# Performance work log

Measured on AMD Instinct MI355X. Metric: run time of the kernel, lower is better.

The kernel has to match this reference:

```python
import jax, jax.numpy as jnp
import numpy as np


def conv1x1(x, W, b):
    # x: [B,C,H,W], W: [O,C], b: [O]  (torch Conv2d 1x1 squeezed)
    return jnp.einsum('oc,bchw->bohw', W, x) + b[None, :, None, None]


def setup_inputs() -> dict:
    key = jax.random.key(0)
    ks = jax.random.split(key, 7)
    B, C, H, W = 8, 256, 32, 32
    s = 1.0 / np.sqrt(C)
    x = jax.random.normal(ks[0], (B, C, H, W), jnp.float32)
    Wq = jax.random.normal(ks[1], (C, C), jnp.float32) * s
    bq = jax.random.normal(ks[2], (C,), jnp.float32) * 0.01
    Wk = jax.random.normal(ks[3], (C, C), jnp.float32) * s
    bk = jax.random.normal(ks[4], (C,), jnp.float32) * 0.01
    Wo = jax.random.normal(ks[5], (C, C), jnp.float32) * s
    bo = jax.random.normal(ks[6], (C,), jnp.float32) * 0.01
    return {"x": x, "Wq": Wq, "bq": bq, "Wk": Wk, "bk": bk, "Wo": Wo, "bo": bo}


def reference(x, Wq, bq, Wk, bk, Wo, bo):
    B, C, H, W = x.shape
    HW = H * W
    scale = 1.0 / (C ** 0.5)
    # proj_query: torch does view(B,C,HW).permute(0,2,1).transpose(1,2).contiguous().view(-1,C)
    # which is a row-major reshape of [B,C,HW] into [B*HW, C] (channel/spatial interleaved).
    # Reproduced faithfully.
    q = conv1x1(x, Wq, bq).reshape(B, C, HW).reshape(-1, C)          # [B*HW, C]
    # proj_key: view(B,C,HW).transpose(0,1).contiguous().view(C,-1) -> true [C, B*HW]
    k = jnp.transpose(conv1x1(x, Wk, bk).reshape(B, C, HW), (1, 0, 2)).reshape(C, -1)
    x_w = (q @ k).reshape(B * HW, B, HW)                              # [BHW, B, HW]
    out_co = jnp.max(x_w, axis=-1) + jnp.mean(x_w, axis=-1)           # [BHW, B]
    x_co = jnp.mean(out_co, axis=-1).reshape(B, HW) * scale           # [B, HW]
    x_co = jax.nn.softmax(x_co, axis=-1).reshape(B, 1, H, W)
    return conv1x1(x * x_co, Wo, bo)
```

## Files before the change

### kernel.cpp

```cpp
#include <hip/hip_runtime.h>

#define BATCH 8
#define CH 256
#define HWSZ 1024
#define BHW 8192

typedef _Float16 f16;
typedef _Float16 f16x4 __attribute__((ext_vector_type(4)));
typedef _Float16 f16x8 __attribute__((ext_vector_type(8)));
typedef float f32x4 __attribute__((ext_vector_type(4)));
typedef unsigned long long u64;
typedef __attribute__((address_space(3))) unsigned int lds_u32;
typedef __attribute__((address_space(1))) const unsigned int glob_u32;

__global__ __launch_bounds__(256) void xmean_kernel(const float* __restrict__ x,
                                                    float* __restrict__ xmean)
{
    const int row  = blockIdx.x * 16 + (threadIdx.x >> 4);
    const int part = threadIdx.x & 15;
    const float4* p = (const float4*)(x + (size_t)row * HWSZ + part * 64);
    float s = 0.f;
#pragma unroll
    for (int i = 0; i < 16; ++i) { float4 v = p[i]; s += v.x + v.y + v.z + v.w; }
    s += __shfl_xor(s, 1, 64);
    s += __shfl_xor(s, 2, 64);
    s += __shfl_xor(s, 4, 64);
    s += __shfl_xor(s, 8, 64);
    if (part == 0) xmean[row] = s * (1.0f / HWSZ);
}

__global__ __launch_bounds__(256) void kmeanW_kernel(
    const float* __restrict__ Wk, const float* __restrict__ bk,
    const float* __restrict__ xmean, float* __restrict__ kmean)
{
    __shared__ float xm[BATCH * CH];
    const int tid = threadIdx.x;
#pragma unroll
    for (int i = 0; i < 8; ++i) xm[i * 256 + tid] = xmean[i * 256 + tid];
    __syncthreads();

    float acc[8];
#pragma unroll
    for (int b = 0; b < 8; ++b) acc[b] = 0.f;
    const float4* w = (const float4*)(Wk + tid * CH);
    for (int c4 = 0; c4 < 64; ++c4) {
        float4 wv = w[c4];
        float wa[4] = {wv.x, wv.y, wv.z, wv.w};
#pragma unroll
        for (int cc = 0; cc < 4; ++cc)
#pragma unroll
            for (int b = 0; b < 8; ++b)
                acc[b] = fmaf(wa[cc], xm[b * 256 + c4 * 4 + cc], acc[b]);
    }
    const float bkv = bk[tid];
#pragma unroll
    for (int b = 0; b < 8; ++b) kmean[b * 256 + tid] = acc[b] + bkv;
}

__global__ __launch_bounds__(256, 2) void pgemm_kernel(
    const float* __restrict__ x,
    const float* __restrict__ Wq, const float* __restrict__ Wk, const float* __restrict__ Wo,
    const float* __restrict__ bq, const float* __restrict__ bk,
    f16* __restrict__ Qh, char* __restrict__ Ksw, float* __restrict__ Yout)
{
    __shared__ __align__(16) char kbuf[32 * 1024];
    __shared__ __align__(16) float xt[256][36];
    f16* tile = (f16*)&xt[0][0];
    char* tileb = (char*)&xt[0][0];

    const int mb   = blockIdx.y;
    const int pxg0 = blockIdx.x * 32;
    const int b    = pxg0 >> 10;
    const int hw0  = pxg0 & 1023;
    const int tid  = threadIdx.x;
    const int lane = tid & 63;
    const int wid  = tid >> 6;
    const int m = lane & 15, g = lane >> 4;

    {
        const int f4 = tid & 7;
        const int cs = tid >> 3;
#pragma unroll
        for (int pass = 0; pass < 8; ++pass) {
            const int c = pass * 32 + cs;
            float4 v = *(const float4*)(x + ((size_t)b * CH + c) * HWSZ + hw0 + f4 * 4);
            *(float4*)&xt[c][f4 * 4] = v;
        }
    }
    __syncthreads();

    {
        const int px = tid & 31;
        const int q8 = tid >> 5;
        const int sw = (px & 7) << 4;
#pragma unroll
        for (int r = 0; r < 4; ++r) {
            f16x8 hi, lo;
#pragma unroll
            for (int i = 0; i < 8; ++i) {
                const int c = q8 * 32 + r * 8 + i;
                float v = xt[c][px];
                f16 h = (f16)v;
                hi[i] = h;
                lo[i] = (f16)(v - (float)h);
            }
            const int base = q8 * 64 + r * 16;
            *(f16x8*)(kbuf + px * 1024 + (base ^ sw)) = hi;
            *(f16x8*)(kbuf + px * 1024 + 512 + (base ^ sw)) = lo;
        }
    }

    const float* Wsel = (mb == 0) ? Wq : (mb == 1) ? Wk : Wo;
    f16x8 a[4][8];
#pragma unroll
    for (int t = 0; t < 4; ++t)
#pragma unroll
        for (int kk = 0; kk < 8; ++kk) {
            const float* wrow = Wsel + (size_t)(wid * 64 + t * 16 + m) * CH + kk * 32 + g * 8;
            float4 w0 = *(const float4*)(wrow);
            float4 w1 = *(const float4*)(wrow + 4);
            f16x8 av;
            av[0] = (f16)w0.x; av[1] = (f16)w0.y; av[2] = (f16)w0.z; av[3] = (f16)w0.w;
            av[4] = (f16)w1.x; av[5] = (f16)w1.y; av[6] = (f16)w1.z; av[7] = (f16)w1.w;
            a[t][kk] = av;
        }

    __syncthreads();

    f32x4 acc[4][2];
    const f32x4 vz = {0.f, 0.f, 0.f, 0.f};
#pragma unroll
    for (int t = 0; t < 4; ++t) { acc[t][0] = vz; acc[t][1] = vz; }

    const int sw0 = (m & 7) << 4;
#pragma unroll
    for (int ks = 0; ks < 16; ++ks) {
        const int X = ks * 64 + g * 16;
        f16x8 b0 = *(const f16x8*)(kbuf + m * 1024 + (X ^ sw0));
        f16x8 b1 = *(const f16x8*)(kbuf + (16 + m) * 1024 + (X ^ sw0));
#pragma unroll
        for (int t = 0; t < 4; ++t) {
            acc[t][0] = __builtin_amdgcn_mfma_f32_16x16x32_f16(a[t][ks & 7], b0, acc[t][0], 0, 0, 0);
            acc[t][1] = __builtin_amdgcn_mfma_f32_16x16x32_f16(a[t][ks & 7], b1, acc[t][1], 0, 0, 0);
        }
    }

    if (mb == 2) {
#pragma unroll
        for (int t = 0; t < 4; ++t)
#pragma unroll
            for (int u = 0; u < 2; ++u)
#pragma unroll
                for (int j = 0; j < 4; ++j) {
                    const int co = wid * 64 + t * 16 + 4 * g + j;
                    Yout[((size_t)b * CH + co) * HWSZ + hw0 + u * 16 + m] = acc[t][u][j];
                }
        return;
    }

    const float* bias = (mb == 0) ? bq : bk;
    if (mb == 0) {
#pragma unroll
        for (int t = 0; t < 4; ++t) {
            const int co0 = wid * 64 + t * 16 + 4 * g;
            float4 bv = *(const float4*)(bias + co0);
            float ba[4] = {bv.x, bv.y, bv.z, bv.w};
#pragma unroll
            for (int u = 0; u < 2; ++u) {
                const int px = u * 16 + m;
#pragma unroll
                for (int j = 0; j < 4; ++j)
                    tile[(co0 + j) * 32 + (px ^ (j << 3))] = (f16)(acc[t][u][j] + ba[j]);
            }
        }
        __syncthreads();
#pragma unroll
        for (int pass = 0; pass < 4; ++pass) {
            const int co  = pass * 64 + (tid >> 2);
            const int run = tid & 3;
            f16x8 v = *(const f16x8*)(tile + co * 32 + ((run * 8) ^ ((co & 3) << 3)));
            *(f16x8*)(Qh + ((size_t)b * CH + co) * HWSZ + hw0 + run * 8) = v;
        }
    } else {
#pragma unroll
        for (int t = 0; t < 4; ++t) {
            const int co0 = wid * 64 + t * 16 + 4 * g;
            float4 bv = *(const float4*)(bias + co0);
            float ba[4] = {bv.x, bv.y, bv.z, bv.w};
#pragma unroll
            for (int u = 0; u < 2; ++u) {
                const int px = u * 16 + m;
                f16x4 pk;
#pragma unroll
                for (int j = 0; j < 4; ++j) pk[j] = (f16)(acc[t][u][j] + ba[j]);
                *(f16x4*)(tileb + px * 512 + ((co0 * 2) ^ (m << 3))) = pk;
            }
        }
        __syncthreads();
        const int px = tid & 31;
        const int rp = tid >> 5;
        const int kloc = (px & 15) << 3;
        const int kglb = (px & 7) << 4;
        char* grow = Ksw + (size_t)(pxg0 + px) * 512;
#pragma unroll
        for (int i = 0; i < 4; ++i) {
            const int r = rp + i * 8;
            u64 a0 = *(const u64*)(tileb + px * 512 + ((r * 16) ^ kloc));
            u64 a1 = *(const u64*)(tileb + px * 512 + ((r * 16 + 8) ^ kloc));
            char* gdst = grow + ((r * 16) ^ kglb);
            *(u64*)gdst = a0;
            *(u64*)(gdst + 8) = a1;
        }
    }
}

__global__ __launch_bounds__(512, 4) void score_kernel(
    const f16* __restrict__ Qh, const char* __restrict__ Ksw, float* __restrict__ rowmax)
{
    __shared__ __align__(16) char kbuf[2][32768];
    __shared__ float lds_rm[128][2];

    const int batch = blockIdx.x & 7;
    const int r0    = (blockIdx.x >> 3) * 128;
    const int tid   = threadIdx.x;
    const int lane  = tid & 63;
    const int wid   = tid >> 6;
    const int wr = wid >> 1, wc = wid & 1;
    const int m = lane & 15, g = lane >> 4;
    const int rbase = r0 + wr * 32;

    const char* kbase = Ksw + (size_t)batch * HWSZ * 512;

#define STAGE(buf, ch)                                                                  \
    {                                                                                   \
        const char* _src = kbase + (ch) * 64 * 512 + tid * 16;                          \
        char* _dst = &kbuf[buf][tid * 16];                                              \
        __builtin_amdgcn_global_load_lds((glob_u32*)(_src),        (lds_u32*)(_dst),        16, 0, 0); \
        __builtin_amdgcn_global_load_lds((glob_u32*)(_src + 8192), (lds_u32*)(_dst + 8192), 16, 0, 0); \
        __builtin_amdgcn_global_load_lds((glob_u32*)(_src + 16384),(lds_u32*)(_dst + 16384),16, 0, 0); \
        __builtin_amdgcn_global_load_lds((glob_u32*)(_src + 24576),(lds_u32*)(_dst + 24576),16, 0, 0); \
    }

    STAGE(0, 0);

    f16x8 a[2][8];
#pragma unroll
    for (int t = 0; t < 2; ++t)
#pragma unroll
        for (int kk = 0; kk < 8; ++kk)
            a[t][kk] = *(const f16x8*)(Qh + (size_t)(rbase + t * 16 + m) * CH + kk * 32 + 8 * g);

    int boff[8][2];
    {
        const int sw = (m & 7) << 4;
#pragma unroll
        for (int kk = 0; kk < 8; ++kk)
#pragma unroll
            for (int u2 = 0; u2 < 2; ++u2) {
                const int col = wc * 32 + u2 * 16 + m;
                boff[kk][u2] = col * 512 + ((kk * 64 + g * 16) ^ sw);
            }
    }

    float rm[2][4];
#pragma unroll
    for (int t = 0; t < 2; ++t)
#pragma unroll
        for (int jj = 0; jj < 4; ++jj) rm[t][jj] = -1e30f;

    __syncthreads();

    int cur = 0;
    for (int ch = 0; ch < 16; ++ch) {
        if (ch < 15) STAGE(cur ^ 1, ch + 1);

        const char* kb = &kbuf[cur][0];
        f32x4 acc[2][2];
        const f32x4 vz = {0.f, 0.f, 0.f, 0.f};
#pragma unroll
        for (int t = 0; t < 2; ++t) { acc[t][0] = vz; acc[t][1] = vz; }

#pragma unroll
        for (int kk = 0; kk < 8; ++kk) {
            f16x8 bfr[2];
            bfr[0] = *(const f16x8*)(kb + boff[kk][0]);
            bfr[1] = *(const f16x8*)(kb + boff[kk][1]);
#pragma unroll
            for (int t = 0; t < 2; ++t) {
                acc[t][0] = __builtin_amdgcn_mfma_f32_16x16x32_f16(a[t][kk], bfr[0], acc[t][0], 0, 0, 0);
                acc[t][1] = __builtin_amdgcn_mfma_f32_16x16x32_f16(a[t][kk], bfr[1], acc[t][1], 0, 0, 0);
            }
        }

#pragma unroll
        for (int t = 0; t < 2; ++t)
#pragma unroll
            for (int jj = 0; jj < 4; ++jj)
                rm[t][jj] = fmaxf(rm[t][jj], fmaxf(acc[t][0][jj], acc[t][1][jj]));

        __syncthreads();
        cur ^= 1;
    }
#undef STAGE

#pragma unroll
    for (int d = 1; d < 16; d <<= 1)
#pragma unroll
        for (int t = 0; t < 2; ++t)
#pragma unroll
            for (int jj = 0; jj < 4; ++jj)
                rm[t][jj] = fmaxf(rm[t][jj], __shfl_xor(rm[t][jj], d, 64));

    if (m == 0) {
#pragma unroll
        for (int t = 0; t < 2; ++t)
#pragma unroll
            for (int jj = 0; jj < 4; ++jj)
                lds_rm[wr * 32 + t * 16 + g * 4 + jj][wc] = rm[t][jj];
    }
    __syncthreads();
    if (tid < 128)
        rowmax[(size_t)(r0 + tid) * BATCH + batch] = fmaxf(lds_rm[tid][0], lds_rm[tid][1]);
}

__global__ __launch_bounds__(256) void logits_kernel(
    const f16* __restrict__ Qh, const float* __restrict__ kmean,
    const float* __restrict__ rowmax, float* __restrict__ logits)
{
    __shared__ float km[BATCH][CH];
    const int tid = threadIdx.x;
#pragma unroll
    for (int i = 0; i < 8; ++i) km[i][tid] = kmean[i * 256 + tid];
    __syncthreads();

    const int r = blockIdx.x * 256 + tid;
    float acc[8];
#pragma unroll
    for (int b = 0; b < 8; ++b) acc[b] = 0.f;

    const f16x8* q = (const f16x8*)(Qh + (size_t)r * CH);
    for (int c8 = 0; c8 < 32; ++c8) {
        f16x8 qv = q[c8];
        float qf[8];
#pragma unroll
        for (int i = 0; i < 8; ++i) qf[i] = (float)qv[i];
#pragma unroll
        for (int b = 0; b < 8; ++b) {
            float4 k0 = *(const float4*)&km[b][c8 * 8];
            float4 k1 = *(const float4*)&km[b][c8 * 8 + 4];
            acc[b] = fmaf(qf[0], k0.x, acc[b]); acc[b] = fmaf(qf[1], k0.y, acc[b]);
            acc[b] = fmaf(qf[2], k0.z, acc[b]); acc[b] = fmaf(qf[3], k0.w, acc[b]);
            acc[b] = fmaf(qf[4], k1.x, acc[b]); acc[b] = fmaf(qf[5], k1.y, acc[b]);
            acc[b] = fmaf(qf[6], k1.z, acc[b]); acc[b] = fmaf(qf[7], k1.w, acc[b]);
        }
    }
    float lg = 0.f;
#pragma unroll
    for (int b = 0; b < 8; ++b) lg += rowmax[(size_t)r * 8 + b] + acc[b];
    logits[r] = lg * (1.0f / 128.0f);
}

__global__ __launch_bounds__(256) void softmax_kernel(const float* __restrict__ logits,
                                                      float* __restrict__ wgt)
{
    const int br = blockIdx.x, tid = threadIdx.x;
    __shared__ float red[256];
    float l[4];
#pragma unroll
    for (int i = 0; i < 4; ++i) l[i] = logits[br * HWSZ + i * 256 + tid];

    float mx = fmaxf(fmaxf(l[0], l[1]), fmaxf(l[2], l[3]));
    red[tid] = mx;
    __syncthreads();
    for (int s = 128; s > 0; s >>= 1) {
        if (tid < s) red[tid] = fmaxf(red[tid], red[tid + s]);
        __syncthreads();
    }
    mx = red[0];
    __syncthreads();

    float e[4], sm = 0.f;
#pragma unroll
    for (int i = 0; i < 4; ++i) { e[i] = expf(l[i] - mx); sm += e[i]; }
    red[tid] = sm;
    __syncthreads();
    for (int s = 128; s > 0; s >>= 1) {
        if (tid < s) red[tid] += red[tid + s];
        __syncthreads();
    }
    const float inv = 1.0f / red[0];
#pragma unroll
    for (int i = 0; i < 4; ++i)
        wgt[br * HWSZ + i * 256 + tid] = e[i] * inv;
}

__global__ __launch_bounds__(256) void gate_kernel(float* __restrict__ out,
                                                   const float* __restrict__ wgt,
                                                   const float* __restrict__ bo)
{
    const size_t idx = ((size_t)blockIdx.x * 256 + threadIdx.x) * 8;
    const int b  = (int)(idx >> 18);
    const int c  = (int)(idx >> 10) & 255;
    const int hw = (int)idx & 1023;

    float4 y0 = *(const float4*)(out + idx);
    float4 y1 = *(const float4*)(out + idx + 4);
    float4 w0 = *(const float4*)(wgt + b * HWSZ + hw);
    float4 w1 = *(const float4*)(wgt + b * HWSZ + hw + 4);
    const float bov = bo[c];

    float4 o0, o1;
    o0.x = fmaf(y0.x, w0.x, bov); o0.y = fmaf(y0.y, w0.y, bov);
    o0.z = fmaf(y0.z, w0.z, bov); o0.w = fmaf(y0.w, w0.w, bov);
    o1.x = fmaf(y1.x, w1.x, bov); o1.y = fmaf(y1.y, w1.y, bov);
    o1.z = fmaf(y1.z, w1.z, bov); o1.w = fmaf(y1.w, w1.w, bov);
    *(float4*)(out + idx)     = o0;
    *(float4*)(out + idx + 4) = o1;
}

extern "C" void kernel_launch(void* const* d_in, const int* in_sizes, int n_in,
                              void* d_out, int out_size, void* d_ws, size_t ws_size,
                              hipStream_t stream)
{
    const float* x  = (const float*)d_in[0];
    const float* Wq = (const float*)d_in[1];
    const float* bq = (const float*)d_in[2];
    const float* Wk = (const float*)d_in[3];
    const float* bk = (const float*)d_in[4];
    const float* Wo = (const float*)d_in[5];
    const float* bo = (const float*)d_in[6];
    float* out = (float*)d_out;

    char* ws = (char*)d_ws;
    f16*   Qh     = (f16*)(ws);
    char*  Ksw    = (char*)(ws + (4 << 20));
    float* rowmax = (float*)(ws + (8 << 20));
    float* kmean  = (float*)(ws + (8 << 20) + (256 << 10));
    float* xmean  = (float*)(ws + (8 << 20) + (264 << 10));
    float* logits = (float*)(ws + (8 << 20) + (272 << 10));
    float* wgt    = (float*)(ws + (8 << 20) + (304 << 10));

    xmean_kernel  <<<dim3(128),     256, 0, stream>>>(x, xmean);
    kmeanW_kernel <<<dim3(1),       256, 0, stream>>>(Wk, bk, xmean, kmean);
    pgemm_kernel  <<<dim3(256, 3),  256, 0, stream>>>(x, Wq, Wk, Wo, bq, bk, Qh, Ksw, out);
    score_kernel  <<<dim3(512),     512, 0, stream>>>(Qh, Ksw, rowmax);
    logits_kernel <<<dim3(32),      256, 0, stream>>>(Qh, kmean, rowmax, logits);
    softmax_kernel<<<dim3(8),       256, 0, stream>>>(logits, wgt);
    gate_kernel   <<<dim3(1024),    256, 0, stream>>>(out, wgt, bo);
}
```

Baseline: 104.5 us.

## Split projection GEMMs, fuse gate into Wo GEMM, retile score kernel

The Wo projection is moved out of the shared projection kernel into a separate kernel that runs after the softmax and applies the gate weight and bias in its epilogue. This removes the separate read-modify-write gate pass over the output, and that GEMM uses only hi fp16 x with a single K pass. The Q and K projections now share one 512-thread block that converts x once and runs two passes. Other changes: the score kernel goes from 512 to 256 threads with 64 rows per wave-row, xmean uses 32 lanes per row, and kmeanW is spread over 8 blocks.

```diff
diff --git a/kernel.cpp b/kernel.cpp
--- a/kernel.cpp
+++ b/kernel.cpp
@@ -16,16 +16,17 @@
 __global__ __launch_bounds__(256) void xmean_kernel(const float* __restrict__ x,
                                                     float* __restrict__ xmean)
 {
-    const int row  = blockIdx.x * 16 + (threadIdx.x >> 4);
-    const int part = threadIdx.x & 15;
-    const float4* p = (const float4*)(x + (size_t)row * HWSZ + part * 64);
+    const int row  = blockIdx.x * 8 + (threadIdx.x >> 5);
+    const int part = threadIdx.x & 31;
+    const float4* p = (const float4*)(x + (size_t)row * HWSZ);
     float s = 0.f;
 #pragma unroll
-    for (int i = 0; i < 16; ++i) { float4 v = p[i]; s += v.x + v.y + v.z + v.w; }
+    for (int i = 0; i < 8; ++i) { float4 v = p[i * 32 + part]; s += v.x + v.y + v.z + v.w; }
     s += __shfl_xor(s, 1, 64);
     s += __shfl_xor(s, 2, 64);
     s += __shfl_xor(s, 4, 64);
     s += __shfl_xor(s, 8, 64);
+    s += __shfl_xor(s, 16, 64);
     if (part == 0) xmean[row] = s * (1.0f / HWSZ);
 }
 
@@ -33,42 +34,35 @@
     const float* __restrict__ Wk, const float* __restrict__ bk,
     const float* __restrict__ xmean, float* __restrict__ kmean)
 {
-    __shared__ float xm[BATCH * CH];
+    __shared__ float xm[CH];
+    const int b = blockIdx.x;
     const int tid = threadIdx.x;
-#pragma unroll
-    for (int i = 0; i < 8; ++i) xm[i * 256 + tid] = xmean[i * 256 + tid];
-    __syncthreads();
-
-    float acc[8];
-#pragma unroll
-    for (int b = 0; b < 8; ++b) acc[b] = 0.f;
+    xm[tid] = xmean[b * 256 + tid];
+    __syncthreads();
+
+    float acc = 0.f;
     const float4* w = (const float4*)(Wk + tid * CH);
     for (int c4 = 0; c4 < 64; ++c4) {
         float4 wv = w[c4];
-        float wa[4] = {wv.x, wv.y, wv.z, wv.w};
-#pragma unroll
-        for (int cc = 0; cc < 4; ++cc)
-#pragma unroll
-            for (int b = 0; b < 8; ++b)
-                acc[b] = fmaf(wa[cc], xm[b * 256 + c4 * 4 + cc], acc[b]);
-    }
-    const float bkv = bk[tid];
-#pragma unroll
-    for (int b = 0; b < 8; ++b) kmean[b * 256 + tid] = acc[b] + bkv;
-}
-
-__global__ __launch_bounds__(256, 2) void pgemm_kernel(
+        acc = fmaf(wv.x, xm[c4 * 4 + 0], acc);
+        acc = fmaf(wv.y, xm[c4 * 4 + 1], acc);
+        acc = fmaf(wv.z, xm[c4 * 4 + 2], acc);
+        acc = fmaf(wv.w, xm[c4 * 4 + 3], acc);
+    }
+    kmean[b * 256 + tid] = acc + bk[tid];
+}
+
+__global__ __launch_bounds__(512, 1) void pgemmQK_kernel(
     const float* __restrict__ x,
-    const float* __restrict__ Wq, const float* __restrict__ Wk, const float* __restrict__ Wo,
+    const float* __restrict__ Wq, const float* __restrict__ Wk,
     const float* __restrict__ bq, const float* __restrict__ bk,
-    f16* __restrict__ Qh, char* __restrict__ Ksw, float* __restrict__ Yout)
+    f16* __restrict__ Qh, char* __restrict__ Ksw)
 {
     __shared__ __align__(16) char kbuf[32 * 1024];
     __shared__ __align__(16) float xt[256][36];
     f16* tile = (f16*)&xt[0][0];
     char* tileb = (char*)&xt[0][0];
 
-    const int mb   = blockIdx.y;
     const int pxg0 = blockIdx.x * 32;
     const int b    = pxg0 >> 10;
     const int hw0  = pxg0 & 1023;
@@ -81,8 +75,8 @@
         const int f4 = tid & 7;
         const int cs = tid >> 3;
 #pragma unroll
-        for (int pass = 0; pass < 8; ++pass) {
-            const int c = pass * 32 + cs;
+        for (int pass = 0; pass < 4; ++pass) {
+            const int c = pass * 64 + cs;
             float4 v = *(const float4*)(x + ((size_t)b * CH + c) * HWSZ + hw0 + f4 * 4);
             *(float4*)&xt[c][f4 * 4] = v;
         }
@@ -94,117 +88,115 @@
         const int q8 = tid >> 5;
         const int sw = (px & 7) << 4;
 #pragma unroll
-        for (int r = 0; r < 4; ++r) {
+        for (int r = 0; r < 2; ++r) {
             f16x8 hi, lo;
 #pragma unroll
             for (int i = 0; i < 8; ++i) {
-                const int c = q8 * 32 + r * 8 + i;
+                const int c = q8 * 16 + r * 8 + i;
                 float v = xt[c][px];
                 f16 h = (f16)v;
                 hi[i] = h;
                 lo[i] = (f16)(v - (float)h);
             }
-            const int base = q8 * 64 + r * 16;
+            const int base = q8 * 32 + r * 16;
             *(f16x8*)(kbuf + px * 1024 + (base ^ sw)) = hi;
             *(f16x8*)(kbuf + px * 1024 + 512 + (base ^ sw)) = lo;
         }
     }
 
-    const float* Wsel = (mb == 0) ? Wq : (mb == 1) ? Wk : Wo;
-    f16x8 a[4][8];
-#pragma unroll
-    for (int t = 0; t < 4; ++t)
-#pragma unroll
-        for (int kk = 0; kk < 8; ++kk) {
-            const float* wrow = Wsel + (size_t)(wid * 64 + t * 16 + m) * CH + kk * 32 + g * 8;
-            float4 w0 = *(const float4*)(wrow);
-            float4 w1 = *(const float4*)(wrow + 4);
-            f16x8 av;
-            av[0] = (f16)w0.x; av[1] = (f16)w0.y; av[2] = (f16)w0.z; av[3] = (f16)w0.w;
-            av[4] = (f16)w1.x; av[5] = (f16)w1.y; av[6] = (f16)w1.z; av[7] = (f16)w1.w;
-            a[t][kk] = av;
-        }
-
-    __syncthreads();
-
-    f32x4 acc[4][2];
+    f16x8 a[2][8];
+#define LOAD_W(Wsel)                                                                     \
+    {                                                                                    \
+        _Pragma("unroll")                                                                \
+        for (int t = 0; t < 2; ++t)                                                      \
+            _Pragma("unroll")                                                            \
+            for (int kk = 0; kk < 8; ++kk) {                                             \
+                const float* wrow = (Wsel) + (size_t)(wid * 32 + t * 16 + m) * CH + kk * 32 + g * 8; \
+                float4 w0 = *(const float4*)(wrow);                                      \
+                float4 w1 = *(const float4*)(wrow + 4);                                  \
+                f16x8 av;                                                                \
+                av[0] = (f16)w0.x; av[1] = (f16)w0.y; av[2] = (f16)w0.z; av[3] = (f16)w0.w; \
+                av[4] = (f16)w1.x; av[5] = (f16)w1.y; av[6] = (f16)w1.z; av[7] = (f16)w1.w; \
+                a[t][kk] = av;                                                           \
+            }                                                                            \
+    }
+    LOAD_W(Wq);
+    __syncthreads();
+
+    const int sw0 = (m & 7) << 4;
     const f32x4 vz = {0.f, 0.f, 0.f, 0.f};
-#pragma unroll
-    for (int t = 0; t < 4; ++t) { acc[t][0] = vz; acc[t][1] = vz; }
-
-    const int sw0 = (m & 7) << 4;
-#pragma unroll
-    for (int ks = 0; ks < 16; ++ks) {
-        const int X = ks * 64 + g * 16;
-        f16x8 b0 = *(const f16x8*)(kbuf + m * 1024 + (X ^ sw0));
-        f16x8 b1 = *(const f16x8*)(kbuf + (16 + m) * 1024 + (X ^ sw0));
-#pragma unroll
-        for (int t = 0; t < 4; ++t) {
-            acc[t][0] = __builtin_amdgcn_mfma_f32_16x16x32_f16(a[t][ks & 7], b0, acc[t][0], 0, 0, 0);
-            acc[t][1] = __builtin_amdgcn_mfma_f32_16x16x32_f16(a[t][ks & 7], b1, acc[t][1], 0, 0, 0);
-        }
-    }
-
-    if (mb == 2) {
-#pragma unroll
-        for (int t = 0; t < 4; ++t)
-#pragma unroll
-            for (int u = 0; u < 2; ++u)
-#pragma unroll
-                for (int j = 0; j < 4; ++j) {
-                    const int co = wid * 64 + t * 16 + 4 * g + j;
-                    Yout[((size_t)b * CH + co) * HWSZ + hw0 + u * 16 + m] = acc[t][u][j];
-                }
-        return;
-    }
-
-    const float* bias = (mb == 0) ? bq : bk;
-    if (mb == 0) {
-#pragma unroll
-        for (int t = 0; t < 4; ++t) {
-            const int co0 = wid * 64 + t * 16 + 4 * g;
-            float4 bv = *(const float4*)(bias + co0);
-            float ba[4] = {bv.x, bv.y, bv.z, bv.w};
-#pragma unroll
-            for (int u = 0; u < 2; ++u) {
-                const int px = u * 16 + m;
-#pragma unroll
-                for (int j = 0; j < 4; ++j)
-                    tile[(co0 + j) * 32 + (px ^ (j << 3))] = (f16)(acc[t][u][j] + ba[j]);
-            }
-        }
-        __syncthreads();
-#pragma unroll
-        for (int pass = 0; pass < 4; ++pass) {
-            const int co  = pass * 64 + (tid >> 2);
-            const int run = tid & 3;
-            f16x8 v = *(const f16x8*)(tile + co * 32 + ((run * 8) ^ ((co & 3) << 3)));
-            *(f16x8*)(Qh + ((size_t)b * CH + co) * HWSZ + hw0 + run * 8) = v;
-        }
-    } else {
-#pragma unroll
-        for (int t = 0; t < 4; ++t) {
-            const int co0 = wid * 64 + t * 16 + 4 * g;
-            float4 bv = *(const float4*)(bias + co0);
-            float ba[4] = {bv.x, bv.y, bv.z, bv.w};
-#pragma unroll
-            for (int u = 0; u < 2; ++u) {
-                const int px = u * 16 + m;
-                f16x4 pk;
-#pragma unroll
-                for (int j = 0; j < 4; ++j) pk[j] = (f16)(acc[t][u][j] + ba[j]);
-                *(f16x4*)(tileb + px * 512 + ((co0 * 2) ^ (m << 3))) = pk;
-            }
-        }
-        __syncthreads();
+    f32x4 acc[2][2];
+
+#define MFMA_PASS()                                                                      \
+    {                                                                                    \
+        _Pragma("unroll")                                                                \
+        for (int t = 0; t < 2; ++t) { acc[t][0] = vz; acc[t][1] = vz; }                  \
+        _Pragma("unroll")                                                                \
+        for (int ks = 0; ks < 16; ++ks) {                                                \
+            const int X = ks * 64 + g * 16;                                              \
+            f16x8 b0 = *(const f16x8*)(kbuf + m * 1024 + (X ^ sw0));                     \
+            f16x8 b1 = *(const f16x8*)(kbuf + (16 + m) * 1024 + (X ^ sw0));              \
+            _Pragma("unroll")                                                            \
+            for (int t = 0; t < 2; ++t) {                                                \
+                acc[t][0] = __builtin_amdgcn_mfma_f32_16x16x32_f16(a[t][ks & 7], b0, acc[t][0], 0, 0, 0); \
+                acc[t][1] = __builtin_amdgcn_mfma_f32_16x16x32_f16(a[t][ks & 7], b1, acc[t][1], 0, 0, 0); \
+            }                                                                            \
+        }                                                                                \
+    }
+
+    MFMA_PASS();
+
+#pragma unroll
+    for (int t = 0; t < 2; ++t) {
+        const int co0 = wid * 32 + t * 16 + 4 * g;
+        float4 bv = *(const float4*)(bq + co0);
+        float ba[4] = {bv.x, bv.y, bv.z, bv.w};
+#pragma unroll
+        for (int u = 0; u < 2; ++u) {
+            const int px = u * 16 + m;
+#pragma unroll
+            for (int j = 0; j < 4; ++j)
+                tile[(co0 + j) * 32 + (px ^ (j << 3))] = (f16)(acc[t][u][j] + ba[j]);
+        }
+    }
+    __syncthreads();
+#pragma unroll
+    for (int pass = 0; pass < 2; ++pass) {
+        const int co  = pass * 128 + (tid >> 2);
+        const int run = tid & 3;
+        f16x8 v = *(const f16x8*)(tile + co * 32 + ((run * 8) ^ ((co & 3) << 3)));
+        *(f16x8*)(Qh + ((size_t)b * CH + co) * HWSZ + hw0 + run * 8) = v;
+    }
+
+    LOAD_W(Wk);
+    MFMA_PASS();
+    __syncthreads();
+
+#pragma unroll
+    for (int t = 0; t < 2; ++t) {
+        const int co0 = wid * 32 + t * 16 + 4 * g;
+        float4 bv = *(const float4*)(bk + co0);
+        float ba[4] = {bv.x, bv.y, bv.z, bv.w};
+#pragma unroll
+        for (int u = 0; u < 2; ++u) {
+            const int px = u * 16 + m;
+            f16x4 pk;
+#pragma unroll
+            for (int j = 0; j < 4; ++j) pk[j] = (f16)(acc[t][u][j] + ba[j]);
+            *(f16x4*)(tileb + px * 512 + ((co0 * 2) ^ (m << 3)));
+            *(f16x4*)(tileb + px * 512 + ((co0 * 2) ^ (m << 3))) = pk;
+        }
+    }
+    __syncthreads();
+    {
         const int px = tid & 31;
         const int rp = tid >> 5;
         const int kloc = (px & 15) << 3;
         const int kglb = (px & 7) << 4;
         char* grow = Ksw + (size_t)(pxg0 + px) * 512;
 #pragma unroll
-        for (int i = 0; i < 4; ++i) {
-            const int r = rp + i * 8;
+        for (int i = 0; i < 2; ++i) {
+            const int r = rp + i * 16;
             u64 a0 = *(const u64*)(tileb + px * 512 + ((r * 16) ^ kloc));
             u64 a1 = *(const u64*)(tileb + px * 512 + ((r * 16 + 8) ^ kloc));
             char* gdst = grow + ((r * 16) ^ kglb);
@@ -212,9 +204,11 @@
             *(u64*)(gdst + 8) = a1;
         }
     }
-}
-
-__global__ __launch_bounds__(512, 4) void score_kernel(
+#undef MFMA_PASS
+#undef LOAD_W
+}
+
+__global__ __launch_bounds__(256, 2) void score_kernel(
     const f16* __restrict__ Qh, const char* __restrict__ Ksw, float* __restrict__ rowmax)
 {
     __shared__ __align__(16) char kbuf[2][32768];
@@ -227,25 +221,25 @@
     const int wid   = tid >> 6;
     const int wr = wid >> 1, wc = wid & 1;
     const int m = lane & 15, g = lane >> 4;
-    const int rbase = r0 + wr * 32;
+    const int rbase = r0 + wr * 64;
 
     const char* kbase = Ksw + (size_t)batch * HWSZ * 512;
 
-#define STAGE(buf, ch)                                                                  \
-    {                                                                                   \
-        const char* _src = kbase + (ch) * 64 * 512 + tid * 16;                          \
-        char* _dst = &kbuf[buf][tid * 16];                                              \
-        __builtin_amdgcn_global_load_lds((glob_u32*)(_src),        (lds_u32*)(_dst),        16, 0, 0); \
-        __builtin_amdgcn_global_load_lds((glob_u32*)(_src + 8192), (lds_u32*)(_dst + 8192), 16, 0, 0); \
-        __builtin_amdgcn_global_load_lds((glob_u32*)(_src + 16384),(lds_u32*)(_dst + 16384),16, 0, 0); \
-        __builtin_amdgcn_global_load_lds((glob_u32*)(_src + 24576),(lds_u32*)(_dst + 24576),16, 0, 0); \
+#define STAGE(buf, ch)                                                                   \
+    {                                                                                    \
+        const char* _src = kbase + (ch) * 64 * 512 + tid * 16;                           \
+        char* _dst = &kbuf[buf][tid * 16];                                               \
+        _Pragma("unroll")                                                                \
+        for (int k = 0; k < 8; ++k)                                                      \
+            __builtin_amdgcn_global_load_lds((glob_u32*)(_src + k * 4096),               \
+                                             (lds_u32*)(_dst + k * 4096), 16, 0, 0);     \
     }
 
     STAGE(0, 0);
 
-    f16x8 a[2][8];
-#pragma unroll
-    for (int t = 0; t < 2; ++t)
+    f16x8 a[4][8];
+#pragma unroll
+    for (int t = 0; t < 4; ++t)
 #pragma unroll
         for (int kk = 0; kk < 8; ++kk)
             a[t][kk] = *(const f16x8*)(Qh + (size_t)(rbase + t * 16 + m) * CH + kk * 32 + 8 * g);
@@ -262,9 +256,9 @@
             }
     }
 
-    float rm[2][4];
-#pragma unroll
-    for (int t = 0; t < 2; ++t)
+    float rm[4][4];
+#pragma unroll
+    for (int t = 0; t < 4; ++t)
 #pragma unroll
         for (int jj = 0; jj < 4; ++jj) rm[t][jj] = -1e30f;
 
@@ -275,10 +269,10 @@
         if (ch < 15) STAGE(cur ^ 1, ch + 1);
 
         const char* kb = &kbuf[cur][0];
-        f32x4 acc[2][2];
+        f32x4 acc[4][2];
         const f32x4 vz = {0.f, 0.f, 0.f, 0.f};
 #pragma unroll
-        for (int t = 0; t < 2; ++t) { acc[t][0] = vz; acc[t][1] = vz; }
+        for (int t = 0; t < 4; ++t) { acc[t][0] = vz; acc[t][1] = vz; }
 
 #pragma unroll
         for (int kk = 0; kk < 8; ++kk) {
@@ -286,14 +280,14 @@
             bfr[0] = *(const f16x8*)(kb + boff[kk][0]);
             bfr[1] = *(const f16x8*)(kb + boff[kk][1]);
 #pragma unroll
-            for (int t = 0; t < 2; ++t) {
+            for (int t = 0; t < 4; ++t) {
                 acc[t][0] = __builtin_amdgcn_mfma_f32_16x16x32_f16(a[t][kk], bfr[0], acc[t][0], 0, 0, 0);
                 acc[t][1] = __builtin_amdgcn_mfma_f32_16x16x32_f16(a[t][kk], bfr[1], acc[t][1], 0, 0, 0);
             }
         }
 
 #pragma unroll
-        for (int t = 0; t < 2; ++t)
+        for (int t = 0; t < 4; ++t)
 #pragma unroll
             for (int jj = 0; jj < 4; ++jj)
                 rm[t][jj] = fmaxf(rm[t][jj], fmaxf(acc[t][0][jj], acc[t][1][jj]));
@@ -306,17 +300,17 @@
 #pragma unroll
     for (int d = 1; d < 16; d <<= 1)
 #pragma unroll
-        for (int t = 0; t < 2; ++t)
+        for (int t = 0; t < 4; ++t)
 #pragma unroll
             for (int jj = 0; jj < 4; ++jj)
                 rm[t][jj] = fmaxf(rm[t][jj], __shfl_xor(rm[t][jj], d, 64));
 
     if (m == 0) {
 #pragma unroll
-        for (int t = 0; t < 2; ++t)
+        for (int t = 0; t < 4; ++t)
 #pragma unroll
             for (int jj = 0; jj < 4; ++jj)
-                lds_rm[wr * 32 + t * 16 + g * 4 + jj][wc] = rm[t][jj];
+                lds_rm[wr * 64 + t * 16 + g * 4 + jj][wc] = rm[t][jj];
     }
     __syncthreads();
     if (tid < 128)
@@ -394,28 +388,96 @@
         wgt[br * HWSZ + i * 256 + tid] = e[i] * inv;
 }
 
-__global__ __launch_bounds__(256) void gate_kernel(float* __restrict__ out,
-                                                   const float* __restrict__ wgt,
-                                                   const float* __restrict__ bo)
-{
-    const size_t idx = ((size_t)blockIdx.x * 256 + threadIdx.x) * 8;
-    const int b  = (int)(idx >> 18);
-    const int c  = (int)(idx >> 10) & 255;
-    const int hw = (int)idx & 1023;
-
-    float4 y0 = *(const float4*)(out + idx);
-    float4 y1 = *(const float4*)(out + idx + 4);
-    float4 w0 = *(const float4*)(wgt + b * HWSZ + hw);
-    float4 w1 = *(const float4*)(wgt + b * HWSZ + hw + 4);
-    const float bov = bo[c];
-
-    float4 o0, o1;
-    o0.x = fmaf(y0.x, w0.x, bov); o0.y = fmaf(y0.y, w0.y, bov);
-    o0.z = fmaf(y0.z, w0.z, bov); o0.w = fmaf(y0.w, w0.w, bov);
-    o1.x = fmaf(y1.x, w1.x, bov); o1.y = fmaf(y1.y, w1.y, bov);
-    o1.z = fmaf(y1.z, w1.z, bov); o1.w = fmaf(y1.w, w1.w, bov);
-    *(float4*)(out + idx)     = o0;
-    *(float4*)(out + idx + 4) = o1;
+__global__ __launch_bounds__(512, 1) void pgemmY_kernel(
+    const float* __restrict__ x, const float* __restrict__ Wo, const float* __restrict__ bo,
+    const float* __restrict__ wgt, float* __restrict__ out)
+{
+    __shared__ __align__(16) char kbuf[16 * 1024];
+    __shared__ __align__(16) float xt[256][36];
+
+    const int pxg0 = blockIdx.x * 32;
+    const int b    = pxg0 >> 10;
+    const int hw0  = pxg0 & 1023;
+    const int tid  = threadIdx.x;
+    const int lane = tid & 63;
+    const int wid  = tid >> 6;
+    const int m = lane & 15, g = lane >> 4;
+
+    {
+        const int f4 = tid & 7;
+        const int cs = tid >> 3;
+#pragma unroll
+        for (int pass = 0; pass < 4; ++pass) {
+            const int c = pass * 64 + cs;
+            float4 v = *(const float4*)(x + ((size_t)b * CH + c) * HWSZ + hw0 + f4 * 4);
+            *(float4*)&xt[c][f4 * 4] = v;
+        }
+    }
+    __syncthreads();
+
+    {
+        const int px = tid & 31;
+        const int q8 = tid >> 5;
+        const int sw = (px & 7) << 4;
+#pragma unroll
+        for (int r = 0; r < 2; ++r) {
+            f16x8 hi;
+#pragma unroll
+            for (int i = 0; i < 8; ++i)
+                hi[i] = (f16)xt[q8 * 16 + r * 8 + i][px];
+            *(f16x8*)(kbuf + px * 512 + ((q8 * 32 + r * 16) ^ sw)) = hi;
+        }
+    }
+
+    f16x8 a[2][8];
+#pragma unroll
+    for (int t = 0; t < 2; ++t)
+#pragma unroll
+        for (int kk = 0; kk < 8; ++kk) {
+            const float* wrow = Wo + (size_t)(wid * 32 + t * 16 + m) * CH + kk * 32 + g * 8;
+            float4 w0 = *(const float4*)(wrow);
+            float4 w1 = *(const float4*)(wrow + 4);
+            f16x8 av;
+            av[0] = (f16)w0.x; av[1] = (f16)w0.y; av[2] = (f16)w0.z; av[3] = (f16)w0.w;
+            av[4] = (f16)w1.x; av[5] = (f16)w1.y; av[6] = (f16)w1.z; av[7] = (f16)w1.w;
+            a[t][kk] = av;
+        }
+
+    __syncthreads();
+
+    f32x4 acc[2][2];
+    const f32x4 vz = {0.f, 0.f, 0.f, 0.f};
+#pragma unroll
+    for (int t = 0; t < 2; ++t) { acc[t][0] = vz; acc[t][1] = vz; }
+
+    const int sw0 = (m & 7) << 4;
+#pragma unroll
+    for (int ks = 0; ks < 8; ++ks) {
+        const int X = ks * 64 + g * 16;
+        f16x8 b0 = *(const f16x8*)(kbuf + m * 512 + (X ^ sw0));
+        f16x8 b1 = *(const f16x8*)(kbuf + (16 + m) * 512 + (X ^ sw0));
+#pragma unroll
+        for (int t = 0; t < 2; ++t) {
+            acc[t][0] = __builtin_amdgcn_mfma_f32_16x16x32_f16(a[t][ks], b0, acc[t][0], 0, 0, 0);
+            acc[t][1] = __builtin_amdgcn_mfma_f32_16x16x32_f16(a[t][ks], b1, acc[t][1], 0, 0, 0);
+        }
+    }
+
+    float wv[2];
+    wv[0] = wgt[b * HWSZ + hw0 + m];
+    wv[1] = wgt[b * HWSZ + hw0 + 16 + m];
+#pragma unroll
+    for (int t = 0; t < 2; ++t) {
+        const int co0 = wid * 32 + t * 16 + 4 * g;
+        float4 bv = *(const float4*)(bo + co0);
+        float ba[4] = {bv.x, bv.y, bv.z, bv.w};
+#pragma unroll
+        for (int u = 0; u < 2; ++u)
+#pragma unroll
+            for (int j = 0; j < 4; ++j)
+                out[((size_t)b * CH + co0 + j) * HWSZ + hw0 + u * 16 + m] =
+                    fmaf(acc[t][u][j], wv[u], ba[j]);
+    }
 }
 
 extern "C" void kernel_launch(void* const* d_in, const int* in_sizes, int n_in,
@@ -440,11 +502,11 @@
     float* logits = (float*)(ws + (8 << 20) + (272 << 10));
     float* wgt    = (float*)(ws + (8 << 20) + (304 << 10));
 
-    xmean_kernel  <<<dim3(128),     256, 0, stream>>>(x, xmean);
-    kmeanW_kernel <<<dim3(1),       256, 0, stream>>>(Wk, bk, xmean, kmean);
-    pgemm_kernel  <<<dim3(256, 3),  256, 0, stream>>>(x, Wq, Wk, Wo, bq, bk, Qh, Ksw, out);
-    score_kernel  <<<dim3(512),     512, 0, stream>>>(Qh, Ksw, rowmax);
-    logits_kernel <<<dim3(32),      256, 0, stream>>>(Qh, kmean, rowmax, logits);
-    softmax_kernel<<<dim3(8),       256, 0, stream>>>(logits, wgt);
-    gate_kernel   <<<dim3(1024),    256, 0, stream>>>(out, wgt, bo);
-}
+    xmean_kernel  <<<dim3(256),  256, 0, stream>>>(x, xmean);
+    kmeanW_kernel <<<dim3(8),    256, 0, stream>>>(Wk, bk, xmean, kmean);
+    pgemmQK_kernel<<<dim3(256),  512, 0, stream>>>(x, Wq, Wk, bq, bk, Qh, Ksw);
+    score_kernel  <<<dim3(512),  256, 0, stream>>>(Qh, Ksw, rowmax);
+    logits_kernel <<<dim3(32),   256, 0, stream>>>(Qh, kmean, rowmax, logits);
+    softmax_kernel<<<dim3(8),    256, 0, stream>>>(logits, wgt);
+    pgemmY_kernel <<<dim3(256),  512, 0, stream>>>(x, Wo, bo, wgt, out);
+}
```

Result: no change. 102.7 us (-1.7%).
